# Performance work log

Hardware: AMD Instinct MI355X
Metric: run time of the kernel (lower is better)

The kernel has to match this reference:

```python
import jax, jax.numpy as jnp
import numpy as np

H = W = 56
WS = 7        # window size
SS = 3        # shift size
NH = 8        # num heads
EPS = 1e-5


def _rel_pos_index(ws):
    coords = np.stack(np.meshgrid(np.arange(ws), np.arange(ws), indexing='ij')).reshape(2, -1)
    rel = (coords[:, :, None] - coords[:, None, :]).transpose(1, 2, 0)  # (N,N,2)
    rel[:, :, 0] += ws - 1
    rel[:, :, 1] += ws - 1
    rel[:, :, 0] *= 2 * ws - 1
    return rel.sum(-1)  # (N,N) int


def _attn_mask(h, w, ws, ss):
    img = np.zeros((h, w))
    sl = (slice(0, -ws), slice(-ws, -ss), slice(-ss, None))
    cnt = 0
    for hs in sl:
        for wsl in sl:
            img[hs, wsl] = cnt
            cnt += 1
    mw = img.reshape(h // ws, ws, w // ws, ws).transpose(0, 2, 1, 3).reshape(-1, ws * ws)  # (nW,N)
    diff = mw[:, None, :] - mw[:, :, None]  # (nW,N,N)
    return np.where(diff != 0, -100.0, 0.0).astype(np.float32)


def _ln(x, w, b):
    m = x.mean(-1, keepdims=True)
    v = ((x - m) ** 2).mean(-1, keepdims=True)
    return (x - m) * jax.lax.rsqrt(v + EPS) * w + b


def setup_inputs() -> dict:
    key = jax.random.key(0)
    ks = jax.random.split(key, 8)
    C = 256
    s = 0.02
    return {
        'x': jax.random.normal(ks[0], (32, H * W, C), jnp.float32),
        'norm1_w': jnp.ones((C,), jnp.float32),
        'norm1_b': jnp.zeros((C,), jnp.float32),
        'qkv_w': jax.random.normal(ks[1], (3 * C, C), jnp.float32) * s,
        'qkv_b': jnp.zeros((3 * C,), jnp.float32),
        'proj_w': jax.random.normal(ks[2], (C, C), jnp.float32) * s,
        'proj_b': jnp.zeros((C,), jnp.float32),
        'rel_bias_table': jax.random.normal(ks[3], (169, NH), jnp.float32) * s,
        'norm2_w': jnp.ones((C,), jnp.float32),
        'norm2_b': jnp.zeros((C,), jnp.float32),
        'fc1_w': jax.random.normal(ks[4], (4 * C, C), jnp.float32) * s,
        'fc1_b': jnp.zeros((4 * C,), jnp.float32),
        'fc2_w': jax.random.normal(ks[5], (C, 4 * C), jnp.float32) * s,
        'fc2_b': jnp.zeros((C,), jnp.float32),
    }


def reference(x, norm1_w, norm1_b, qkv_w, qkv_b, proj_w, proj_b, rel_bias_table,
              norm2_w, norm2_b, fc1_w, fc1_b, fc2_w, fc2_b):
    B, L, C = x.shape
    N = WS * WS
    nW = (H // WS) * (W // WS)
    hd = C // NH
    scale = hd ** (-0.5)

    rel_idx = jnp.asarray(_rel_pos_index(WS))          # (N,N)
    mask = jnp.asarray(_attn_mask(H, W, WS, SS))       # (nW,N,N)

    shortcut = x
    h = _ln(x, norm1_w, norm1_b).reshape(B, H, W, C)
    h = jnp.roll(h, (-SS, -SS), axis=(1, 2))
    # window partition -> (B*nW, N, C)
    hw = h.reshape(B, H // WS, WS, W // WS, WS, C).transpose(0, 1, 3, 2, 4, 5).reshape(-1, N, C)

    qkv = hw @ qkv_w.T + qkv_b                          # (B_, N, 3C)
    qkv = qkv.reshape(-1, N, 3, NH, hd).transpose(2, 0, 3, 1, 4)
    q, k, v = qkv[0] * scale, qkv[1], qkv[2]            # (B_, NH, N, hd)

    attn = jnp.einsum('bhnd,bhmd->bhnm', q, k)          # (B_, NH, N, N)
    bias = rel_bias_table[rel_idx.reshape(-1)].reshape(N, N, NH).transpose(2, 0, 1)
    attn = attn + bias[None]
    attn = attn.reshape(B, nW, NH, N, N) + mask[None, :, None]
    attn = jax.nn.softmax(attn.reshape(-1, NH, N, N), axis=-1)

    out = jnp.einsum('bhnm,bhmd->bhnd', attn, v)        # (B_, NH, N, hd)
    out = out.transpose(0, 2, 1, 3).reshape(-1, N, C)
    out = out @ proj_w.T + proj_b

    # window reverse + unshift
    out = out.reshape(B, H // WS, W // WS, WS, WS, C).transpose(0, 1, 3, 2, 4, 5).reshape(B, H, W, C)
    out = jnp.roll(out, (SS, SS), axis=(1, 2)).reshape(B, L, C)

    x = shortcut + out
    y = _ln(x, norm2_w, norm2_b)
    y = jax.nn.gelu(y @ fc1_w.T + fc1_b, approximate=False) @ fc2_w.T + fc2_b
    return x + y
```

## Files before the change

kernel.cpp:

```cpp
#include <hip/hip_runtime.h>
#include <hip/hip_bf16.h>
#include <cstddef>

using bf16 = __hip_bfloat16;
typedef __bf16 bf16x8 __attribute__((ext_vector_type(8)));
typedef float f32x4 __attribute__((ext_vector_type(4)));

typedef __attribute__((address_space(1))) const void* gas1_t;
typedef __attribute__((address_space(3))) void* las3_t;

__device__ __forceinline__ void g2lds16(const void* g, void* l) {
  __builtin_amdgcn_global_load_lds((gas1_t)g, (las3_t)l, 16, 0, 0);
}

#define M_ROWS 100352
#define CDIM   256

__global__ void cvt_bf16(const float* __restrict__ in, bf16* __restrict__ out, int n) {
  int i = blockIdx.x * 256 + threadIdx.x;
  if (i < n) out[i] = __float2bfloat16(in[i]);
}

__global__ __launch_bounds__(256) void ln1_shift_kernel(
    const float* __restrict__ x, const float* __restrict__ w, const float* __restrict__ bb,
    bf16* __restrict__ hw) {
  int row = blockIdx.x * 4 + (threadIdx.x >> 6);
  int l = threadIdx.x & 63;
  int b_ = row / 49;
  int n  = row - b_ * 49;
  int bidx = b_ >> 6;
  int wi = b_ & 63;
  int wh = wi >> 3, ww = wi & 7;
  int r = n / 7, c = n - r * 7;
  int y = wh * 7 + r + 3;  if (y >= 56) y -= 56;
  int xx = ww * 7 + c + 3; if (xx >= 56) xx -= 56;
  size_t src = ((size_t)bidx * 3136 + (size_t)(y * 56 + xx)) * 256 + l * 4;
  float4 v = *reinterpret_cast<const float4*>(x + src);
  float s  = v.x + v.y + v.z + v.w;
  float ss = v.x * v.x + v.y * v.y + v.z * v.z + v.w * v.w;
#pragma unroll
  for (int off = 32; off > 0; off >>= 1) {
    s  += __shfl_xor(s, off);
    ss += __shfl_xor(ss, off);
  }
  float mean = s * (1.f / 256.f);
  float var  = ss * (1.f / 256.f) - mean * mean;
  float rs   = rsqrtf(var + 1e-5f);
  int ch = l * 4;
  float4 wv = *reinterpret_cast<const float4*>(w + ch);
  float4 bv = *reinterpret_cast<const float4*>(bb + ch);
  bf16 o[4];
  o[0] = __float2bfloat16((v.x - mean) * rs * wv.x + bv.x);
  o[1] = __float2bfloat16((v.y - mean) * rs * wv.y + bv.y);
  o[2] = __float2bfloat16((v.z - mean) * rs * wv.z + bv.z);
  o[3] = __float2bfloat16((v.w - mean) * rs * wv.w + bv.w);
  *reinterpret_cast<short4*>(hw + (size_t)row * 256 + ch) = *reinterpret_cast<const short4*>(o);
}

__global__ __launch_bounds__(256) void ln_kernel(
    const float* __restrict__ xin, const float* __restrict__ w, const float* __restrict__ bb,
    bf16* __restrict__ out) {
  int row = blockIdx.x * 4 + (threadIdx.x >> 6);
  int l = threadIdx.x & 63;
  size_t src = (size_t)row * 256 + l * 4;
  float4 v = *reinterpret_cast<const float4*>(xin + src);
  float s  = v.x + v.y + v.z + v.w;
  float ss = v.x * v.x + v.y * v.y + v.z * v.z + v.w * v.w;
#pragma unroll
  for (int off = 32; off > 0; off >>= 1) {
    s  += __shfl_xor(s, off);
    ss += __shfl_xor(ss, off);
  }
  float mean = s * (1.f / 256.f);
  float var  = ss * (1.f / 256.f) - mean * mean;
  float rs   = rsqrtf(var + 1e-5f);
  int ch = l * 4;
  float4 wv = *reinterpret_cast<const float4*>(w + ch);
  float4 bv = *reinterpret_cast<const float4*>(bb + ch);
  bf16 o[4];
  o[0] = __float2bfloat16((v.x - mean) * rs * wv.x + bv.x);
  o[1] = __float2bfloat16((v.y - mean) * rs * wv.y + bv.y);
  o[2] = __float2bfloat16((v.z - mean) * rs * wv.z + bv.z);
  o[3] = __float2bfloat16((v.w - mean) * rs * wv.w + bv.w);
  *reinterpret_cast<short4*>(out + src) = *reinterpret_cast<const short4*>(o);
}

__global__ __launch_bounds__(256) void attn_mfma_kernel(
    const bf16* __restrict__ qkv, const float* __restrict__ bias_table,
    bf16* __restrict__ attn_out) {
  __shared__ char smem[4 * 12992];
  const int tid = threadIdx.x;
  const int wid = tid >> 6;
  const int lane = tid & 63;
  const int lrow = lane & 15;
  const int kseg = lane >> 4;
  const int b_ = blockIdx.x >> 1;
  const int h = ((blockIdx.x & 1) << 2) + wid;
  const int wi = b_ & 63;
  const int wh = wi >> 3, ww = wi & 7;

  char* L = smem + wid * 12992;

  const bf16* src0 = qkv + (size_t)b_ * (49 * 768) + h * 32;
#pragma unroll
  for (int t = 0; t < 2; ++t) {
    const bf16* src = src0 + t * 256;
    char* dst = L + t * 4096;
#pragma unroll
    for (int it = 0; it < 4; ++it) {
      int c = it * 64 + lane;
      if (c < 196)
        g2lds16(src + (size_t)(c >> 2) * 768 + (((c & 3) ^ ((c >> 3) & 3)) * 8), dst + c * 16);
    }
  }
  {
    const bf16* src = src0 + 512;
    char* dst = L + 8192;
#pragma unroll
    for (int it = 0; it < 4; ++it) {
      int c = it * 64 + lane;
      if (c < 196)
        g2lds16(src + (size_t)(c >> 2) * 768 + (c & 3) * 8, dst + c * 16);
    }
  }
  if (lane < 60) {
    int4 z = {0, 0, 0, 0};
    *reinterpret_cast<int4*>(L + 8192 + (196 + lane) * 16) = z;
  }
  float* blds = reinterpret_cast<float*>(L + 12288);
  for (int e = lane; e < 169; e += 64) blds[e] = bias_table[e * 8 + h];

  asm volatile("s_waitcnt vmcnt(0) lgkmcnt(0)" ::: "memory");

  const int swb = (kseg ^ ((lrow >> 1) & 3)) * 16;
  bf16x8 qf[4], kf[4];
#pragma unroll
  for (int im = 0; im < 4; ++im)
    qf[im] = *reinterpret_cast<const bf16x8*>(L + (16 * im + lrow) * 64 + swb);
#pragma unroll
  for (int jn = 0; jn < 4; ++jn)
    kf[jn] = *reinterpret_cast<const bf16x8*>(L + 4096 + (16 * jn + lrow) * 64 + swb);
  f32x4 S[4][4] = {};
#pragma unroll
  for (int im = 0; im < 4; ++im)
#pragma unroll
    for (int jn = 0; jn < 4; ++jn)
      S[im][jn] = __builtin_amdgcn_mfma_f32_16x16x32_bf16(qf[im], kf[jn], S[im][jn], 0, 0, 0);

  const float scale = 0.17677669529663689f;
  int fj[4], rj[4], cj[4];
  bool jbad[4];
#pragma unroll
  for (int jn = 0; jn < 4; ++jn) {
    int j = 16 * jn + lrow;
    int rr = (j * 37) >> 8;
    int cc = j - rr * 7;
    rj[jn] = rr; cj[jn] = cc;
    int yj = wh * 7 + rr, xj = ww * 7 + cc;
    fj[jn] = (yj < 49 ? 0 : (yj < 53 ? 1 : 2)) * 3 + (xj < 49 ? 0 : (xj < 53 ? 1 : 2));
    jbad[jn] = (j >= 49);
  }
#pragma unroll
  for (int im = 0; im < 4; ++im) {
#pragma unroll
    for (int r = 0; r < 4; ++r) {
      int i = 16 * im + 4 * kseg + r;
      int ri = (i * 37) >> 8;
      int ci = i - ri * 7;
      int yi = wh * 7 + ri, xi = ww * 7 + ci;
      int fi = (yi < 49 ? 0 : (yi < 53 ? 1 : 2)) * 3 + (xi < 49 ? 0 : (xi < 53 ? 1 : 2));
#pragma unroll
      for (int jn = 0; jn < 4; ++jn) {
        float s = S[im][jn][r] * scale + blds[(ri - rj[jn] + 6) * 13 + (ci - cj[jn] + 6)];
        S[im][jn][r] = (fi != fj[jn] || jbad[jn]) ? -1e30f : s;
      }
    }
  }

#pragma unroll
  for (int im = 0; im < 4; ++im) {
#pragma unroll
    for (int r = 0; r < 4; ++r) {
      float m = fmaxf(fmaxf(S[im][0][r], S[im][1][r]), fmaxf(S[im][2][r], S[im][3][r]));
      m = fmaxf(m, __shfl_xor(m, 1));
      m = fmaxf(m, __shfl_xor(m, 2));
      m = fmaxf(m, __shfl_xor(m, 4));
      m = fmaxf(m, __shfl_xor(m, 8));
      float e0 = __expf(S[im][0][r] - m);
      float e1 = __expf(S[im][1][r] - m);
      float e2 = __expf(S[im][2][r] - m);
      float e3 = __expf(S[im][3][r] - m);
      float sum = e0 + e1 + e2 + e3;
      sum += __shfl_xor(sum, 1);
      sum += __shfl_xor(sum, 2);
      sum += __shfl_xor(sum, 4);
      sum += __shfl_xor(sum, 8);
      float inv = 1.f / sum;
      int i = 16 * im + 4 * kseg + r;
      int xorv = (i & 7) << 4;
      float ev[4] = {e0, e1, e2, e3};
#pragma unroll
      for (int jn = 0; jn < 4; ++jn) {
        bf16 pb = __float2bfloat16(ev[jn] * inv);
        *reinterpret_cast<unsigned short*>(L + i * 128 + (((16 * jn + lrow) * 2) ^ xorv)) =
            *reinterpret_cast<unsigned short*>(&pb);
      }
    }
  }

  f32x4 O[4][2] = {};
#pragma unroll
  for (int ks = 0; ks < 2; ++ks) {
    bf16x8 pa[4];
#pragma unroll
    for (int im = 0; im < 4; ++im) {
      int row = 16 * im + lrow;
      int byte = (ks * 64 + kseg * 16) ^ ((row & 7) << 4);
      pa[im] = *reinterpret_cast<const bf16x8*>(L + row * 128 + byte);
    }
#pragma unroll
    for (int dn = 0; dn < 2; ++dn) {
      bf16x8 vf;
#pragma unroll
      for (int jj = 0; jj < 8; ++jj) {
        int j = ks * 32 + kseg * 8 + jj;
        reinterpret_cast<unsigned short*>(&vf)[jj] =
            *reinterpret_cast<const unsigned short*>(L + 8192 + j * 64 + (16 * dn + lrow) * 2);
      }
#pragma unroll
      for (int im = 0; im < 4; ++im)
        O[im][dn] = __builtin_amdgcn_mfma_f32_16x16x32_bf16(pa[im], vf, O[im][dn], 0, 0, 0);
    }
  }

  bf16* outb = attn_out + (size_t)b_ * 49 * 256 + h * 32;
#pragma unroll
  for (int im = 0; im < 4; ++im) {
#pragma unroll
    for (int r = 0; r < 4; ++r) {
      int i = 16 * im + 4 * kseg + r;
      if (i < 49) {
#pragma unroll
        for (int dn = 0; dn < 2; ++dn)
          outb[(size_t)i * 256 + 16 * dn + lrow] = __float2bfloat16(O[im][dn][r]);
      }
    }
  }
}

enum { EPI_BF16 = 0, EPI_GELU = 1, EPI_PROJ = 2, EPI_ADD = 3 };

template <int EPI>
__global__ __launch_bounds__(256) void gemm_kernel(
    const bf16* __restrict__ A, const bf16* __restrict__ Bw,
    const float* __restrict__ bias, int NY, int N, int K,
    void* __restrict__ outp, const float* __restrict__ addf) {
  __shared__ __align__(16) bf16 As[3][128][32];
  __shared__ __align__(16) bf16 Bs[3][128][32];
  __shared__ int tdst[128];

  const int tid = threadIdx.x;
  const int bid = blockIdx.x;
  const int nblk = gridDim.x;
  const int w = (bid & 7) * (nblk >> 3) + (bid >> 3);
  const int bx = w / NY;
  const int by = w - bx * NY;
  const int m0 = bx * 128;
  const int n0 = by * 128;

  if constexpr (EPI == EPI_PROJ) {
    if (tid < 128) {
      int m = m0 + tid;
      int b_ = m / 49;
      int n = m - b_ * 49;
      int bidx = b_ >> 6;
      int wi = b_ & 63;
      int wh = wi >> 3, ww = wi & 7;
      int r = n / 7, c = n - r * 7;
      int y = wh * 7 + r + 3;  if (y >= 56) y -= 56;
      int xx = ww * 7 + c + 3; if (xx >= 56) xx -= 56;
      tdst[tid] = bidx * 3136 + y * 56 + xx;
    }
  }

  const int wv = tid >> 6;
  const int wm = wv >> 1, wn = wv & 1;
  const int l = tid & 63;
  const int lrow = l & 15;
  const int kseg = l >> 4;
  const int sw = (kseg ^ ((lrow >> 1) & 3)) * 8;

  f32x4 acc[4][4] = {};

  const int nk = K >> 5;

  auto stage = [&](int buf, int kt) {
    int k0 = kt << 5;
#pragma unroll
    for (int i = 0; i < 2; ++i) {
      int idx = i * 256 + tid;
      int col = ((idx & 3) ^ ((idx >> 3) & 3)) * 8;
      g2lds16(A + (size_t)(m0 + (idx >> 2)) * K + (k0 + col),
              (char*)(&As[buf][0][0]) + idx * 16);
    }
#pragma unroll
    for (int i = 0; i < 2; ++i) {
      int idx = i * 256 + tid;
      int col = ((idx & 3) ^ ((idx >> 3) & 3)) * 8;
      g2lds16(Bw + (size_t)(n0 + (idx >> 2)) * K + (k0 + col),
              (char*)(&Bs[buf][0][0]) + idx * 16);
    }
  };

  stage(0, 0);
  stage(1, 1);

  int cur = 0;
  for (int kt = 0; kt < nk; ++kt) {
    if (kt + 2 < nk) stage((cur + 2) % 3, kt + 2);

    if (kt + 2 < nk)      asm volatile("s_waitcnt vmcnt(8)" ::: "memory");
    else if (kt + 1 < nk) asm volatile("s_waitcnt vmcnt(4)" ::: "memory");
    else                  asm volatile("s_waitcnt vmcnt(0)" ::: "memory");
    __builtin_amdgcn_s_barrier();
    asm volatile("" ::: "memory");

    bf16x8 af[4], bfr[4];
#pragma unroll
    for (int im = 0; im < 4; ++im)
      af[im] = *reinterpret_cast<const bf16x8*>(&As[cur][wm * 64 + im * 16 + lrow][sw]);
#pragma unroll
    for (int in_ = 0; in_ < 4; ++in_)
      bfr[in_] = *reinterpret_cast<const bf16x8*>(&Bs[cur][wn * 64 + in_ * 16 + lrow][sw]);
#pragma unroll
    for (int im = 0; im < 4; ++im)
#pragma unroll
      for (int in_ = 0; in_ < 4; ++in_)
        acc[im][in_] = __builtin_amdgcn_mfma_f32_16x16x32_bf16(af[im], bfr[in_], acc[im][in_], 0, 0, 0);

    asm volatile("" ::: "memory");
    __builtin_amdgcn_s_barrier();
    cur = (cur + 1) % 3;
  }

  const int col = l & 15;
#pragma unroll
  for (int im = 0; im < 4; ++im) {
#pragma unroll
    for (int in_ = 0; in_ < 4; ++in_) {
      int nch = n0 + wn * 64 + in_ * 16 + col;
      float bv = bias[nch];
#pragma unroll
      for (int r = 0; r < 4; ++r) {
        int m = m0 + wm * 64 + im * 16 + (l >> 4) * 4 + r;
        float val = acc[im][in_][r] + bv;
        if constexpr (EPI == EPI_BF16) {
          ((bf16*)outp)[(size_t)m * N + nch] = __float2bfloat16(val);
        } else if constexpr (EPI == EPI_GELU) {
          float u = val;
          float yv = 0.7978845608028654f * (u + 0.044715f * u * u * u);
          float e = __expf(2.f * yv);
          float th = 1.f - 2.f / (e + 1.f);
          val = 0.5f * u * (1.f + th);
          ((bf16*)outp)[(size_t)m * N + nch] = __float2bfloat16(val);
        } else if constexpr (EPI == EPI_PROJ) {
          int td = tdst[m - m0];
          size_t o = (size_t)td * 256 + nch;
          ((float*)outp)[o] = addf[o] + val;
        } else {
          size_t o = (size_t)m * N + nch;
          ((float*)outp)[o] = addf[o] + val;
        }
      }
    }
  }
}

extern "C" void kernel_launch(void* const* d_in, const int* in_sizes, int n_in,
                              void* d_out, int out_size, void* d_ws, size_t ws_size,
                              hipStream_t stream) {
  const float* x      = (const float*)d_in[0];
  const float* n1w    = (const float*)d_in[1];
  const float* n1b    = (const float*)d_in[2];
  const float* qkv_w  = (const float*)d_in[3];
  const float* qkv_b  = (const float*)d_in[4];
  const float* proj_w = (const float*)d_in[5];
  const float* proj_b = (const float*)d_in[6];
  const float* relb   = (const float*)d_in[7];
  const float* n2w    = (const float*)d_in[8];
  const float* n2b    = (const float*)d_in[9];
  const float* fc1_w  = (const float*)d_in[10];
  const float* fc1_b  = (const float*)d_in[11];
  const float* fc2_w  = (const float*)d_in[12];
  const float* fc2_b  = (const float*)d_in[13];
  float* out = (float*)d_out;
  char* ws = (char*)d_ws;

  const size_t HW_BYTES   = (size_t)M_ROWS * 256 * 2;
  const size_t QKV_BYTES  = (size_t)M_ROWS * 768 * 2;
  const size_t YIN_BYTES  = (size_t)M_ROWS * 256 * 2;

  char* regA = ws;
  bf16* hw    = (bf16*)regA;
  bf16* qkvb  = (bf16*)(regA + HW_BYTES);
  bf16* h1    = (bf16*)regA;
  char* p = regA + HW_BYTES + QKV_BYTES;
  bf16* y_in   = (bf16*)p;             p += YIN_BYTES;
  bf16* wq  = (bf16*)p;                p += (size_t)768 * 256 * 2;
  bf16* wp  = (bf16*)p;                p += (size_t)256 * 256 * 2;
  bf16* wf1 = (bf16*)p;                p += (size_t)1024 * 256 * 2;
  bf16* wf2 = (bf16*)p;                p += (size_t)256 * 1024 * 2;
  float* x_new = out;
  (void)ws_size; (void)in_sizes; (void)n_in; (void)out_size;

  cvt_bf16<<<768, 256, 0, stream>>>(qkv_w, wq, 768 * 256);
  cvt_bf16<<<256, 256, 0, stream>>>(proj_w, wp, 256 * 256);
  cvt_bf16<<<1024, 256, 0, stream>>>(fc1_w, wf1, 1024 * 256);
  cvt_bf16<<<1024, 256, 0, stream>>>(fc2_w, wf2, 256 * 1024);

  ln1_shift_kernel<<<M_ROWS / 4, 256, 0, stream>>>(x, n1w, n1b, hw);

  gemm_kernel<EPI_BF16><<<784 * 6, 256, 0, stream>>>(hw, wq, qkv_b, 6, 768, 256, qkvb, nullptr);

  attn_mfma_kernel<<<4096, 256, 0, stream>>>(qkvb, relb, hw);

  gemm_kernel<EPI_PROJ><<<784 * 2, 256, 0, stream>>>(hw, wp, proj_b, 2, 256, 256, x_new, x);

  ln_kernel<<<M_ROWS / 4, 256, 0, stream>>>(x_new, n2w, n2b, y_in);

  gemm_kernel<EPI_GELU><<<784 * 8, 256, 0, stream>>>(y_in, wf1, fc1_b, 8, 1024, 256, h1, nullptr);

  gemm_kernel<EPI_ADD><<<784 * 2, 256, 0, stream>>>(h1, wf2, fc2_b, 2, 256, 1024, out, x_new);
}
```

Measured before the change: 546.1 us.

## Drop LDS staging in GEMM and load MFMA fragments directly from global

```diff
diff --git a/kernel.cpp b/kernel.cpp
--- a/kernel.cpp
+++ b/kernel.cpp
@@ -250,15 +250,11 @@
 
 enum { EPI_BF16 = 0, EPI_GELU = 1, EPI_PROJ = 2, EPI_ADD = 3 };
 
-template <int EPI>
+template <int EPI, int K>
 __global__ __launch_bounds__(256) void gemm_kernel(
     const bf16* __restrict__ A, const bf16* __restrict__ Bw,
-    const float* __restrict__ bias, int NY, int N, int K,
+    const float* __restrict__ bias, int NY, int N,
     void* __restrict__ outp, const float* __restrict__ addf) {
-  __shared__ __align__(16) bf16 As[3][128][32];
-  __shared__ __align__(16) bf16 Bs[3][128][32];
-  __shared__ int tdst[128];
-
   const int tid = threadIdx.x;
   const int bid = blockIdx.x;
   const int nblk = gridDim.x;
@@ -268,92 +264,64 @@
   const int m0 = bx * 128;
   const int n0 = by * 128;
 
-  if constexpr (EPI == EPI_PROJ) {
-    if (tid < 128) {
-      int m = m0 + tid;
-      int b_ = m / 49;
-      int n = m - b_ * 49;
-      int bidx = b_ >> 6;
-      int wi = b_ & 63;
-      int wh = wi >> 3, ww = wi & 7;
-      int r = n / 7, c = n - r * 7;
-      int y = wh * 7 + r + 3;  if (y >= 56) y -= 56;
-      int xx = ww * 7 + c + 3; if (xx >= 56) xx -= 56;
-      tdst[tid] = bidx * 3136 + y * 56 + xx;
-    }
-  }
-
   const int wv = tid >> 6;
   const int wm = wv >> 1, wn = wv & 1;
   const int l = tid & 63;
   const int lrow = l & 15;
   const int kseg = l >> 4;
-  const int sw = (kseg ^ ((lrow >> 1) & 3)) * 8;
+
+  const bf16* Ab[4];
+  const bf16* Bb[4];
+#pragma unroll
+  for (int im = 0; im < 4; ++im)
+    Ab[im] = A + (size_t)(m0 + wm * 64 + im * 16 + lrow) * K + kseg * 8;
+#pragma unroll
+  for (int in_ = 0; in_ < 4; ++in_)
+    Bb[in_] = Bw + (size_t)(n0 + wn * 64 + in_ * 16 + lrow) * K + kseg * 8;
 
   f32x4 acc[4][4] = {};
 
-  const int nk = K >> 5;
-
-  auto stage = [&](int buf, int kt) {
-    int k0 = kt << 5;
-#pragma unroll
-    for (int i = 0; i < 2; ++i) {
-      int idx = i * 256 + tid;
-      int col = ((idx & 3) ^ ((idx >> 3) & 3)) * 8;
-      g2lds16(A + (size_t)(m0 + (idx >> 2)) * K + (k0 + col),
-              (char*)(&As[buf][0][0]) + idx * 16);
-    }
-#pragma unroll
-    for (int i = 0; i < 2; ++i) {
-      int idx = i * 256 + tid;
-      int col = ((idx & 3) ^ ((idx >> 3) & 3)) * 8;
-      g2lds16(Bw + (size_t)(n0 + (idx >> 2)) * K + (k0 + col),
-              (char*)(&Bs[buf][0][0]) + idx * 16);
-    }
-  };
-
-  stage(0, 0);
-  stage(1, 1);
-
-  int cur = 0;
-  for (int kt = 0; kt < nk; ++kt) {
-    if (kt + 2 < nk) stage((cur + 2) % 3, kt + 2);
-
-    if (kt + 2 < nk)      asm volatile("s_waitcnt vmcnt(8)" ::: "memory");
-    else if (kt + 1 < nk) asm volatile("s_waitcnt vmcnt(4)" ::: "memory");
-    else                  asm volatile("s_waitcnt vmcnt(0)" ::: "memory");
-    __builtin_amdgcn_s_barrier();
-    asm volatile("" ::: "memory");
-
-    bf16x8 af[4], bfr[4];
-#pragma unroll
-    for (int im = 0; im < 4; ++im)
-      af[im] = *reinterpret_cast<const bf16x8*>(&As[cur][wm * 64 + im * 16 + lrow][sw]);
-#pragma unroll
-    for (int in_ = 0; in_ < 4; ++in_)
-      bfr[in_] = *reinterpret_cast<const bf16x8*>(&Bs[cur][wn * 64 + in_ * 16 + lrow][sw]);
-#pragma unroll
-    for (int im = 0; im < 4; ++im)
+  for (int k0 = 0; k0 < K; k0 += 128) {
+#pragma unroll
+    for (int kk = 0; kk < 4; ++kk) {
+      const int k = k0 + kk * 32;
+      bf16x8 af[4], bfr[4];
+#pragma unroll
+      for (int im = 0; im < 4; ++im)
+        af[im] = *reinterpret_cast<const bf16x8*>(Ab[im] + k);
 #pragma unroll
       for (int in_ = 0; in_ < 4; ++in_)
-        acc[im][in_] = __builtin_amdgcn_mfma_f32_16x16x32_bf16(af[im], bfr[in_], acc[im][in_], 0, 0, 0);
-
-    asm volatile("" ::: "memory");
-    __builtin_amdgcn_s_barrier();
-    cur = (cur + 1) % 3;
+        bfr[in_] = *reinterpret_cast<const bf16x8*>(Bb[in_] + k);
+#pragma unroll
+      for (int im = 0; im < 4; ++im)
+#pragma unroll
+        for (int in_ = 0; in_ < 4; ++in_)
+          acc[im][in_] = __builtin_amdgcn_mfma_f32_16x16x32_bf16(af[im], bfr[in_], acc[im][in_], 0, 0, 0);
+    }
   }
 
   const int col = l & 15;
 #pragma unroll
   for (int im = 0; im < 4; ++im) {
 #pragma unroll
-    for (int in_ = 0; in_ < 4; ++in_) {
-      int nch = n0 + wn * 64 + in_ * 16 + col;
-      float bv = bias[nch];
-#pragma unroll
-      for (int r = 0; r < 4; ++r) {
-        int m = m0 + wm * 64 + im * 16 + (l >> 4) * 4 + r;
-        float val = acc[im][in_][r] + bv;
+    for (int r = 0; r < 4; ++r) {
+      int m = m0 + wm * 64 + im * 16 + kseg * 4 + r;
+      int td = 0;
+      if constexpr (EPI == EPI_PROJ) {
+        int b_ = m / 49;
+        int n = m - b_ * 49;
+        int bidx = b_ >> 6;
+        int wi = b_ & 63;
+        int wh2 = wi >> 3, ww2 = wi & 7;
+        int rr = n / 7, cc = n - rr * 7;
+        int y = wh2 * 7 + rr + 3;  if (y >= 56) y -= 56;
+        int xx = ww2 * 7 + cc + 3; if (xx >= 56) xx -= 56;
+        td = bidx * 3136 + y * 56 + xx;
+      }
+#pragma unroll
+      for (int in_ = 0; in_ < 4; ++in_) {
+        int nch = n0 + wn * 64 + in_ * 16 + col;
+        float val = acc[im][in_][r] + bias[nch];
         if constexpr (EPI == EPI_BF16) {
           ((bf16*)outp)[(size_t)m * N + nch] = __float2bfloat16(val);
         } else if constexpr (EPI == EPI_GELU) {
@@ -364,7 +332,6 @@
           val = 0.5f * u * (1.f + th);
           ((bf16*)outp)[(size_t)m * N + nch] = __float2bfloat16(val);
         } else if constexpr (EPI == EPI_PROJ) {
-          int td = tdst[m - m0];
           size_t o = (size_t)td * 256 + nch;
           ((float*)outp)[o] = addf[o] + val;
         } else {
@@ -420,15 +387,15 @@
 
   ln1_shift_kernel<<<M_ROWS / 4, 256, 0, stream>>>(x, n1w, n1b, hw);
 
-  gemm_kernel<EPI_BF16><<<784 * 6, 256, 0, stream>>>(hw, wq, qkv_b, 6, 768, 256, qkvb, nullptr);
+  gemm_kernel<EPI_BF16, 256><<<784 * 6, 256, 0, stream>>>(hw, wq, qkv_b, 6, 768, qkvb, nullptr);
 
   attn_mfma_kernel<<<4096, 256, 0, stream>>>(qkvb, relb, hw);
 
-  gemm_kernel<EPI_PROJ><<<784 * 2, 256, 0, stream>>>(hw, wp, proj_b, 2, 256, 256, x_new, x);
+  gemm_kernel<EPI_PROJ, 256><<<784 * 2, 256, 0, stream>>>(hw, wp, proj_b, 2, 256, x_new, x);
 
   ln_kernel<<<M_ROWS / 4, 256, 0, stream>>>(x_new, n2w, n2b, y_in);
 
-  gemm_kernel<EPI_GELU><<<784 * 8, 256, 0, stream>>>(y_in, wf1, fc1_b, 8, 1024, 256, h1, nullptr);
-
-  gemm_kernel<EPI_ADD><<<784 * 2, 256, 0, stream>>>(h1, wf2, fc2_b, 2, 256, 1024, out, x_new);
-}
+  gemm_kernel<EPI_GELU, 256><<<784 * 8, 256, 0, stream>>>(y_in, wf1, fc1_b, 8, 1024, h1, nullptr);
+
+  gemm_kernel<EPI_ADD, 1024><<<784 * 2, 256, 0, stream>>>(h1, wf2, fc2_b, 2, 256, out, x_new);
+}
```

Result: slower. 908.8 us (+66.4%).

## Add B-resident persistent GEMM for K=256 layers processing eight M-tiles per block

Applied to the files above, without the earlier changes.

```diff
diff --git a/kernel.cpp b/kernel.cpp
--- a/kernel.cpp
+++ b/kernel.cpp
@@ -14,7 +14,6 @@
 }
 
 #define M_ROWS 100352
-#define CDIM   256
 
 __global__ void cvt_bf16(const float* __restrict__ in, bf16* __restrict__ out, int n) {
   int i = blockIdx.x * 256 + threadIdx.x;
@@ -250,6 +249,135 @@
 
 enum { EPI_BF16 = 0, EPI_GELU = 1, EPI_PROJ = 2, EPI_ADD = 3 };
 
+__device__ __forceinline__ void epi_store(int EPI, int m, int nch, int N, float val,
+                                          void* outp, const float* addf) {
+  if (EPI == EPI_BF16) {
+    ((bf16*)outp)[(size_t)m * N + nch] = __float2bfloat16(val);
+  } else if (EPI == EPI_GELU) {
+    float u = val;
+    float yv = 0.7978845608028654f * (u + 0.044715f * u * u * u);
+    float e = __expf(2.f * yv);
+    float th = 1.f - 2.f / (e + 1.f);
+    val = 0.5f * u * (1.f + th);
+    ((bf16*)outp)[(size_t)m * N + nch] = __float2bfloat16(val);
+  } else if (EPI == EPI_PROJ) {
+    int b_ = m / 49;
+    int n = m - b_ * 49;
+    int bidx = b_ >> 6;
+    int wi = b_ & 63;
+    int wh2 = wi >> 3, ww2 = wi & 7;
+    int rr = n / 7, cc = n - rr * 7;
+    int y = wh2 * 7 + rr + 3;  if (y >= 56) y -= 56;
+    int xx = ww2 * 7 + cc + 3; if (xx >= 56) xx -= 56;
+    int td = bidx * 3136 + y * 56 + xx;
+    size_t o = (size_t)td * 256 + nch;
+    ((float*)outp)[o] = addf[o] + val;
+  } else {
+    size_t o = (size_t)m * N + nch;
+    ((float*)outp)[o] = addf[o] + val;
+  }
+}
+
+template <int EPI, int NSLICE>
+__global__ __launch_bounds__(256) void bres_gemm(
+    const bf16* __restrict__ A, const bf16* __restrict__ Bw,
+    const float* __restrict__ bias, int N,
+    void* __restrict__ outp, const float* __restrict__ addf) {
+  constexpr int K = 256;
+  __shared__ __align__(16) bf16 Bs[128][K];
+  __shared__ __align__(16) bf16 As[2][128][32];
+
+  const int tid = threadIdx.x;
+  const int slice = blockIdx.x % NSLICE;
+  const int idx   = blockIdx.x / NSLICE;
+  const int n0 = slice * 128;
+
+  const int wv = tid >> 6;
+  const int wm = wv >> 1, wn = wv & 1;
+  const int l = tid & 63;
+  const int lrow = l & 15;
+  const int kseg = l >> 4;
+  const int slot = kseg ^ ((lrow >> 1) & 3);
+
+#pragma unroll
+  for (int i = 0; i < 16; ++i) {
+    int u = i * 256 + tid;
+    int row = u >> 5;
+    int c16 = u & 31;
+    int kt = c16 >> 2, sl = c16 & 3;
+    int col = kt * 32 + (sl ^ ((row >> 1) & 3)) * 8;
+    g2lds16(Bw + (size_t)(n0 + row) * K + col, (char*)(&Bs[0][0]) + u * 16);
+  }
+
+  auto stageA = [&](int buf, int s, int kt) {
+    const bf16* Ab = A + (size_t)(idx * 8 + s) * 128 * K;
+#pragma unroll
+    for (int i = 0; i < 2; ++i) {
+      int u = i * 256 + tid;
+      int row = u >> 2, sl = u & 3;
+      int col = (kt << 5) + (sl ^ ((row >> 1) & 3)) * 8;
+      g2lds16(Ab + (size_t)row * K + col, (char*)(&As[buf][0][0]) + u * 16);
+    }
+  };
+
+  stageA(0, 0, 0);
+
+  f32x4 acc[4][4];
+  const int T = 8 * 8;
+  int buf = 0;
+  for (int t = 0; t < T; ++t) {
+    const int s = t >> 3, kt = t & 7;
+    if (t + 1 < T) {
+      stageA(buf ^ 1, (t + 1) >> 3, (t + 1) & 7);
+      asm volatile("s_waitcnt vmcnt(2)" ::: "memory");
+    } else {
+      asm volatile("s_waitcnt vmcnt(0)" ::: "memory");
+    }
+    __builtin_amdgcn_s_barrier();
+    asm volatile("" ::: "memory");
+
+    if (kt == 0) {
+#pragma unroll
+      for (int a = 0; a < 4; ++a)
+#pragma unroll
+        for (int b = 0; b < 4; ++b) acc[a][b] = f32x4{0.f, 0.f, 0.f, 0.f};
+    }
+
+    bf16x8 af[4], bfr[4];
+#pragma unroll
+    for (int im = 0; im < 4; ++im)
+      af[im] = *reinterpret_cast<const bf16x8*>((char*)(&As[buf][0][0]) + (wm * 64 + im * 16 + lrow) * 64 + slot * 16);
+#pragma unroll
+    for (int in_ = 0; in_ < 4; ++in_)
+      bfr[in_] = *reinterpret_cast<const bf16x8*>((char*)(&Bs[0][0]) + (size_t)(wn * 64 + in_ * 16 + lrow) * 512 + kt * 64 + slot * 16);
+#pragma unroll
+    for (int im = 0; im < 4; ++im)
+#pragma unroll
+      for (int in_ = 0; in_ < 4; ++in_)
+        acc[im][in_] = __builtin_amdgcn_mfma_f32_16x16x32_bf16(af[im], bfr[in_], acc[im][in_], 0, 0, 0);
+
+    asm volatile("" ::: "memory");
+    __builtin_amdgcn_s_barrier();
+    buf ^= 1;
+
+    if (kt == 7) {
+      const int mrow = (idx * 8 + s) * 128;
+#pragma unroll
+      for (int im = 0; im < 4; ++im) {
+#pragma unroll
+        for (int r = 0; r < 4; ++r) {
+          int m = mrow + wm * 64 + im * 16 + kseg * 4 + r;
+#pragma unroll
+          for (int in_ = 0; in_ < 4; ++in_) {
+            int nch = n0 + wn * 64 + in_ * 16 + lrow;
+            epi_store(EPI, m, nch, N, acc[im][in_][r] + bias[nch], outp, addf);
+          }
+        }
+      }
+    }
+  }
+}
+
 template <int EPI>
 __global__ __launch_bounds__(256) void gemm_kernel(
     const bf16* __restrict__ A, const bf16* __restrict__ Bw,
@@ -257,7 +385,6 @@
     void* __restrict__ outp, const float* __restrict__ addf) {
   __shared__ __align__(16) bf16 As[3][128][32];
   __shared__ __align__(16) bf16 Bs[3][128][32];
-  __shared__ int tdst[128];
 
   const int tid = threadIdx.x;
   const int bid = blockIdx.x;
@@ -268,21 +395,6 @@
   const int m0 = bx * 128;
   const int n0 = by * 128;
 
-  if constexpr (EPI == EPI_PROJ) {
-    if (tid < 128) {
-      int m = m0 + tid;
-      int b_ = m / 49;
-      int n = m - b_ * 49;
-      int bidx = b_ >> 6;
-      int wi = b_ & 63;
-      int wh = wi >> 3, ww = wi & 7;
-      int r = n / 7, c = n - r * 7;
-      int y = wh * 7 + r + 3;  if (y >= 56) y -= 56;
-      int xx = ww * 7 + c + 3; if (xx >= 56) xx -= 56;
-      tdst[tid] = bidx * 3136 + y * 56 + xx;
-    }
-  }
-
   const int wv = tid >> 6;
   const int wm = wv >> 1, wn = wv & 1;
   const int l = tid & 63;
@@ -291,7 +403,6 @@
   const int sw = (kseg ^ ((lrow >> 1) & 3)) * 8;
 
   f32x4 acc[4][4] = {};
-
   const int nk = K >> 5;
 
   auto stage = [&](int buf, int kt) {
@@ -343,34 +454,15 @@
     cur = (cur + 1) % 3;
   }
 
-  const int col = l & 15;
 #pragma unroll
   for (int im = 0; im < 4; ++im) {
 #pragma unroll
-    for (int in_ = 0; in_ < 4; ++in_) {
-      int nch = n0 + wn * 64 + in_ * 16 + col;
-      float bv = bias[nch];
-#pragma unroll
-      for (int r = 0; r < 4; ++r) {
-        int m = m0 + wm * 64 + im * 16 + (l >> 4) * 4 + r;
-        float val = acc[im][in_][r] + bv;
-        if constexpr (EPI == EPI_BF16) {
-          ((bf16*)outp)[(size_t)m * N + nch] = __float2bfloat16(val);
-        } else if constexpr (EPI == EPI_GELU) {
-          float u = val;
-          float yv = 0.7978845608028654f * (u + 0.044715f * u * u * u);
-          float e = __expf(2.f * yv);
-          float th = 1.f - 2.f / (e + 1.f);
-          val = 0.5f * u * (1.f + th);
-          ((bf16*)outp)[(size_t)m * N + nch] = __float2bfloat16(val);
-        } else if constexpr (EPI == EPI_PROJ) {
-          int td = tdst[m - m0];
-          size_t o = (size_t)td * 256 + nch;
-          ((float*)outp)[o] = addf[o] + val;
-        } else {
-          size_t o = (size_t)m * N + nch;
-          ((float*)outp)[o] = addf[o] + val;
-        }
+    for (int r = 0; r < 4; ++r) {
+      int m = m0 + wm * 64 + im * 16 + kseg * 4 + r;
+#pragma unroll
+      for (int in_ = 0; in_ < 4; ++in_) {
+        int nch = n0 + wn * 64 + in_ * 16 + lrow;
+        epi_store(EPI, m, nch, N, acc[im][in_][r] + bias[nch], outp, addf);
       }
     }
   }
@@ -420,15 +512,15 @@
 
   ln1_shift_kernel<<<M_ROWS / 4, 256, 0, stream>>>(x, n1w, n1b, hw);
 
-  gemm_kernel<EPI_BF16><<<784 * 6, 256, 0, stream>>>(hw, wq, qkv_b, 6, 768, 256, qkvb, nullptr);
+  bres_gemm<EPI_BF16, 6><<<6 * 98, 256, 0, stream>>>(hw, wq, qkv_b, 768, qkvb, nullptr);
 
   attn_mfma_kernel<<<4096, 256, 0, stream>>>(qkvb, relb, hw);
 
-  gemm_kernel<EPI_PROJ><<<784 * 2, 256, 0, stream>>>(hw, wp, proj_b, 2, 256, 256, x_new, x);
+  bres_gemm<EPI_PROJ, 2><<<2 * 98, 256, 0, stream>>>(hw, wp, proj_b, 256, x_new, x);
 
   ln_kernel<<<M_ROWS / 4, 256, 0, stream>>>(x_new, n2w, n2b, y_in);
 
-  gemm_kernel<EPI_GELU><<<784 * 8, 256, 0, stream>>>(y_in, wf1, fc1_b, 8, 1024, 256, h1, nullptr);
+  bres_gemm<EPI_GELU, 8><<<8 * 98, 256, 0, stream>>>(y_in, wf1, fc1_b, 1024, h1, nullptr);
 
   gemm_kernel<EPI_ADD><<<784 * 2, 256, 0, stream>>>(h1, wf2, fc2_b, 2, 256, 1024, out, x_new);
 }
```

After: 709.4 us. +29.9%, slower.
